# Performance work log

Hardware: AMD Instinct MI355X
Metric: run time of the kernel (lower is better)

Reference implementation:

```python
import jax, jax.numpy as jnp
import numpy as np

L, S, D = 2, 2048, 2048          # layers, seq_len, model dim
H, KVH, HD = 16, 4, 128          # heads, kv heads, head_dim (scale 128**0.5 is hardcoded in source)
F = 8192                         # ffn hidden
EPS = 1e-5
THETA = 500000.0                 # Llama-3 rope base


def setup_inputs() -> dict:
    key = jax.random.key(0)
    ks = jax.random.split(key, 9)
    sc = 0.02
    x = jax.random.normal(ks[0], (S, D), jnp.float32)
    inv_freq = 1.0 / (THETA ** (jnp.arange(0, HD, 2, dtype=jnp.float32) / HD))  # [HD/2]
    ang = jnp.arange(S, dtype=jnp.float32)[:, None] * inv_freq[None, :]         # [S, HD/2]
    w = lambda k, shape: jax.random.normal(k, shape, jnp.float32) * sc
    return {
        "token_embeddings_unnormal": x,
        "freqs_cos": jnp.cos(ang),
        "freqs_sin": jnp.sin(ang),
        "attn_norm_w": jnp.ones((L, D), jnp.float32),
        "wq": w(ks[1], (L, D, D)),
        "wk": w(ks[2], (L, KVH * HD, D)),
        "wv": w(ks[3], (L, KVH * HD, D)),
        "wo": w(ks[4], (L, D, D)),
        "ffn_norm_w": jnp.ones((L, D), jnp.float32),
        "w1": w(ks[5], (L, F, D)),
        "w2": w(ks[6], (L, D, F)),
        "w3": w(ks[7], (L, F, D)),
    }


def _rms_norm(x, w):
    # x * rsqrt(mean(x^2) + eps) * w  (matches source exactly)
    return x * jax.lax.rsqrt(jnp.mean(x * x, axis=-1, keepdims=True) + EPS) * w


def _rope(t, cos, sin):
    # t: [S, h, HD]; complex rotation of consecutive pairs by freqs_cis
    tp = t.reshape(t.shape[0], t.shape[1], HD // 2, 2)
    t0, t1 = tp[..., 0], tp[..., 1]
    c, s = cos[:, None, :], sin[:, None, :]
    return jnp.stack([t0 * c - t1 * s, t0 * s + t1 * c], axis=-1).reshape(t.shape)


def reference(token_embeddings_unnormal, freqs_cos, freqs_sin, attn_norm_w,
              wq, wk, wv, wo, ffn_norm_w, w1, w2, w3):
    x = token_embeddings_unnormal
    scale = 1.0 / np.sqrt(128.0)
    causal = jnp.tril(jnp.ones((S, S), bool))
    for l in range(L):
        h = _rms_norm(x, attn_norm_w[l])
        # batched per-head projections (source loops over heads; same math)
        q = jnp.einsum('sd,hed->she', h, wq[l].reshape(H, HD, D))
        k = jnp.einsum('sd,hed->she', h, wk[l].reshape(KVH, HD, D))
        v = jnp.einsum('sd,hed->she', h, wv[l].reshape(KVH, HD, D))
        q = _rope(q, freqs_cos, freqs_sin)
        k = _rope(k, freqs_cos, freqs_sin)
        # GQA: head `i` uses kv head i // 4
        k = jnp.repeat(k, H // KVH, axis=1)
        v = jnp.repeat(v, H // KVH, axis=1)
        scores = jnp.einsum('she,the->hst', q, k) * scale
        scores = jnp.where(causal[None], scores, -jnp.inf)
        probs = jax.nn.softmax(scores, axis=-1).astype(jnp.bfloat16).astype(jnp.float32)
        attn = jnp.einsum('hst,the->she', probs, v).reshape(S, H * HD)
        x = x + attn @ wo[l].T
        hf = _rms_norm(x, ffn_norm_w[l])
        x = x + (jax.nn.silu(hf @ w1[l].T) * (hf @ w3[l].T)) @ w2[l].T
    return x
```

## Files before the change

kernel.cpp:

```cpp
#include <hip/hip_runtime.h>

#define SLEN 2048
#define DM   2048
#define NH   16
#define NKVH 4
#define HD   128
#define KVD  512
#define FF   8192
#define NLAYER 2
#define EPSV 1e-5f

typedef unsigned short bhalf;
typedef __attribute__((__ext_vector_type__(8))) __bf16 bf16x8;
typedef __attribute__((__ext_vector_type__(4))) float f32x4;

__device__ __forceinline__ float b2f(bhalf u) {
  union { unsigned int i; float f; } v; v.i = ((unsigned int)u) << 16; return v.f;
}
__device__ __forceinline__ bhalf f2b(float f) {
  unsigned int x = __float_as_uint(f);
  return (bhalf)((x + 0x7fffu + ((x >> 16) & 1u)) >> 16);
}

typedef __attribute__((address_space(1))) const void gas_cvoid;
typedef __attribute__((address_space(3))) void las_void;
__device__ __forceinline__ void gload16(const void* g, void* l) {
  __builtin_amdgcn_global_load_lds((gas_cvoid*)g, (las_void*)l, 16, 0, 0);
}
__device__ __forceinline__ f32x4 mfma16(bf16x8 a, bf16x8 b, f32x4 c) {
  return __builtin_amdgcn_mfma_f32_16x16x32_bf16(a, b, c, 0, 0, 0);
}

__global__ __launch_bounds__(256)
void cvt_f32_bf16(const float* __restrict__ in, bhalf* __restrict__ out, size_t n) {
  size_t i = ((size_t)blockIdx.x * 256 + threadIdx.x) * 8;
  const size_t stride = (size_t)gridDim.x * 256 * 8;
  for (; i < n; i += stride) {
    float4 a = *(const float4*)(in + i);
    float4 b = *(const float4*)(in + i + 4);
    int4 o; bhalf* t = (bhalf*)&o;
    t[0]=f2b(a.x); t[1]=f2b(a.y); t[2]=f2b(a.z); t[3]=f2b(a.w);
    t[4]=f2b(b.x); t[5]=f2b(b.y); t[6]=f2b(b.z); t[7]=f2b(b.w);
    *(int4*)(out + i) = o;
  }
}

__global__ __launch_bounds__(256)
void rmsnorm_k(const float* __restrict__ x, const float* __restrict__ w,
               bhalf* __restrict__ out) {
  const int row = blockIdx.x;
  const int tid = threadIdx.x;
  const float4* xr = (const float4*)(x + (size_t)row * DM);
  float4 a = xr[tid*2], b = xr[tid*2 + 1];
  float ss = a.x*a.x + a.y*a.y + a.z*a.z + a.w*a.w
           + b.x*b.x + b.y*b.y + b.z*b.z + b.w*b.w;
  #pragma unroll
  for (int off = 32; off > 0; off >>= 1) ss += __shfl_down(ss, off);
  __shared__ float red[5];
  const int wv = tid >> 6, l = tid & 63;
  if (l == 0) red[wv] = ss;
  __syncthreads();
  if (tid == 0) red[4] = rsqrtf((red[0]+red[1]+red[2]+red[3]) * (1.0f/DM) + EPSV);
  __syncthreads();
  const float rs = red[4];
  const float* wp = w + tid*8;
  float vals[8] = {a.x,a.y,a.z,a.w,b.x,b.y,b.z,b.w};
  int4 o; bhalf* t = (bhalf*)&o;
  #pragma unroll
  for (int j = 0; j < 8; ++j) t[j] = f2b(vals[j] * rs * wp[j]);
  *(int4*)(out + (size_t)row*DM + tid*8) = o;
}

__global__ __launch_bounds__(256)
void rope_k(bhalf* __restrict__ t, const float* __restrict__ c,
            const float* __restrict__ s, int nheads) {
  const int idx = blockIdx.x * 256 + threadIdx.x;
  const int j  = idx & 63;
  const int hh = (idx >> 6) % nheads;
  const int sp = idx / (nheads * 64);
  const float cv = c[sp*64 + j], sv = s[sp*64 + j];
  unsigned int* p = (unsigned int*)(t + ((size_t)sp*nheads + hh)*HD + 2*j);
  const unsigned int pv = *p;
  const float t0 = b2f((bhalf)(pv & 0xffffu)), t1 = b2f((bhalf)(pv >> 16));
  const float o0 = t0*cv - t1*sv, o1 = t0*sv + t1*cv;
  *p = (unsigned int)f2b(o0) | ((unsigned int)f2b(o1) << 16);
}

template<int EPI>
__global__ __launch_bounds__(256, 2)
void gemm_bt(const bhalf* __restrict__ A, const bhalf* __restrict__ B,
             const int N, const int K,
             const bhalf* __restrict__ gate,
             float* __restrict__ outf, bhalf* __restrict__ outb) {
  __shared__ bhalf As[128*32];
  __shared__ bhalf Bs[128*32];
  const int tid = threadIdx.x;
  const int w = tid >> 6, l = tid & 63;
  const int l15 = l & 15, lg = l >> 4;
  const int ntn = N >> 7;
  const int nblocks = gridDim.x;
  const int qq = nblocks >> 3, rr = nblocks & 7;
  const int xcd = blockIdx.x & 7, loc = blockIdx.x >> 3;
  const int swz = (xcd < rr) ? (xcd*(qq+1) + loc) : (rr*(qq+1) + (xcd-rr)*qq + loc);
  const size_t m0 = (size_t)(swz / ntn) << 7;
  const size_t n0 = (size_t)(swz % ntn) << 7;
  f32x4 acc[4][4] = {};
  const int wr = w >> 1, wc = w & 1;
  const int stgrow = l >> 2;
  const int stgcol = (l & 3) << 3;
  const int nk = K >> 5;
  for (int kt = 0; kt < nk; ++kt) {
    const int k0 = kt << 5;
    #pragma unroll
    for (int it = 0; it < 2; ++it) {
      const int c = it*4 + w;
      const int row = c*16 + stgrow;
      gload16(&A[(m0 + row)*K + k0 + stgcol], &As[c*512]);
      gload16(&B[(n0 + row)*K + k0 + stgcol], &Bs[c*512]);
    }
    __syncthreads();
    bf16x8 af[4], bfr[4];
    #pragma unroll
    for (int m = 0; m < 4; ++m)
      af[m] = *(const bf16x8*)&As[(wr*64 + m*16 + l15)*32 + lg*8];
    #pragma unroll
    for (int n = 0; n < 4; ++n)
      bfr[n] = *(const bf16x8*)&Bs[(wc*64 + n*16 + l15)*32 + lg*8];
    #pragma unroll
    for (int m = 0; m < 4; ++m)
      #pragma unroll
      for (int n = 0; n < 4; ++n)
        acc[m][n] = mfma16(af[m], bfr[n], acc[m][n]);
    __syncthreads();
  }
  #pragma unroll
  for (int m = 0; m < 4; ++m) {
    const size_t row = m0 + wr*64 + m*16 + lg*4;
    #pragma unroll
    for (int n = 0; n < 4; ++n) {
      const size_t col = n0 + wc*64 + n*16 + l15;
      #pragma unroll
      for (int r2 = 0; r2 < 4; ++r2) {
        const size_t idx = (row + r2)*(size_t)N + col;
        const float v = acc[m][n][r2];
        if constexpr (EPI == 1) {
          outb[idx] = f2b(v);
        } else if constexpr (EPI == 2) {
          outf[idx] += v;
        } else {
          const float g = b2f(gate[idx]);
          const float si = g / (1.0f + __expf(-g));
          outb[idx] = f2b(si * v);
        }
      }
    }
  }
}

template<int EPI>
__global__ __launch_bounds__(512, 2)
void gemm256(const bhalf* __restrict__ A, const bhalf* __restrict__ B,
             const int N, const int lda, const int klen,
             const bhalf* __restrict__ gate, float* __restrict__ outf,
             bhalf* __restrict__ outb) {
  __shared__ __align__(16) bhalf As[3][256*32];
  __shared__ __align__(16) bhalf Bs[3][256*32];
  const int tid = threadIdx.x;
  const int w = tid >> 6, l = tid & 63;
  const int l15 = l & 15, lg = l >> 4;
  const int rdswz = (l15 >> 1) & 3;
  const int wr = w >> 2, wc = w & 3;
  const int ntn = N >> 8;
  const int nblocks = gridDim.x;
  const int qq = nblocks >> 3, rr = nblocks & 7;
  const int xcd = blockIdx.x & 7, loc = blockIdx.x >> 3;
  const int sb = (xcd < rr) ? (xcd*(qq+1) + loc) : (rr*(qq+1) + (xcd-rr)*qq + loc);
  const size_t m0 = (size_t)(sb / ntn) << 8;
  const size_t n0 = (size_t)(sb % ntn) << 8;
  const int k0 = blockIdx.y * klen;
  const int nk = klen >> 5;
  const int srow = l >> 2;
  const int scol = ((l & 3) ^ ((l >> 3) & 3)) << 3;
  const bhalf* Ag = A + m0 * (size_t)lda + k0;
  const bhalf* Bg = B + n0 * (size_t)lda + k0;

  auto stage = [&](int kt, int buf) {
    #pragma unroll
    for (int r = 0; r < 2; ++r) {
      const int chunk = r*8 + w;
      const size_t go = (size_t)(chunk*16 + srow)*lda + kt*32 + scol;
      gload16(Ag + go, &As[buf][chunk*512]);
      gload16(Bg + go, &Bs[buf][chunk*512]);
    }
  };

  f32x4 acc[8][4] = {};
  auto compute = [&](int cb) {
    const bhalf* Ab = As[cb];
    const bhalf* Bb = Bs[cb];
    const int co = (lg ^ rdswz) << 3;
    bf16x8 bfr[4], am[4];
    #pragma unroll
    for (int n = 0; n < 4; ++n)
      bfr[n] = *(const bf16x8*)&Bb[(wc*64 + n*16 + l15)*32 + co];
    #pragma unroll
    for (int m = 0; m < 4; ++m)
      am[m] = *(const bf16x8*)&Ab[(wr*128 + m*16 + l15)*32 + co];
    __builtin_amdgcn_s_setprio(1);
    #pragma unroll
    for (int m = 0; m < 4; ++m)
      #pragma unroll
      for (int n = 0; n < 4; ++n)
        acc[m][n] = mfma16(am[m], bfr[n], acc[m][n]);
    __builtin_amdgcn_s_setprio(0);
    #pragma unroll
    for (int m = 0; m < 4; ++m)
      am[m] = *(const bf16x8*)&Ab[(wr*128 + 64 + m*16 + l15)*32 + co];
    __builtin_amdgcn_s_setprio(1);
    #pragma unroll
    for (int m = 0; m < 4; ++m)
      #pragma unroll
      for (int n = 0; n < 4; ++n)
        acc[m + 4][n] = mfma16(am[m], bfr[n], acc[m + 4][n]);
    __builtin_amdgcn_s_setprio(0);
  };

  stage(0, 0);
  stage(1, 1);
  asm volatile("s_waitcnt vmcnt(4)" ::: "memory");
  __builtin_amdgcn_s_barrier();
  asm volatile("" ::: "memory");

  int cb = 0, pb = 2;
  for (int kt = 0; kt < nk - 2; ++kt) {
    stage(kt + 2, pb);
    compute(cb);
    asm volatile("s_waitcnt vmcnt(4)" ::: "memory");
    __builtin_amdgcn_s_barrier();
    asm volatile("" ::: "memory");
    cb = (cb + 1 == 3) ? 0 : cb + 1;
    pb = (pb + 1 == 3) ? 0 : pb + 1;
  }
  compute(cb);
  asm volatile("s_waitcnt vmcnt(0)" ::: "memory");
  __builtin_amdgcn_s_barrier();
  asm volatile("" ::: "memory");
  cb = (cb + 1 == 3) ? 0 : cb + 1;
  compute(cb);

  #pragma unroll
  for (int m = 0; m < 8; ++m) {
    const size_t row = m0 + wr*128 + m*16 + lg*4;
    #pragma unroll
    for (int n = 0; n < 4; ++n) {
      const size_t col = n0 + wc*64 + n*16 + l15;
      #pragma unroll
      for (int r2 = 0; r2 < 4; ++r2) {
        const size_t idx = (row + r2) * (size_t)N + col;
        const float v = acc[m][n][r2];
        if constexpr (EPI == 1) {
          outb[idx] = f2b(v);
        } else if constexpr (EPI == 2) {
          outf[idx] += v;
        } else if constexpr (EPI == 3) {
          const float g = b2f(gate[idx]);
          outb[idx] = f2b((g / (1.0f + __expf(-g))) * v);
        } else {
          atomicAdd(&outf[idx], v);
        }
      }
    }
  }
}

__global__ __launch_bounds__(256, 2)
void attn_k(const bhalf* __restrict__ qb, const bhalf* __restrict__ kb,
            const bhalf* __restrict__ vb, bhalf* __restrict__ ob) {
  __shared__ bhalf Ks[64][144];
  __shared__ bhalf Vt[128][80];
  __shared__ bhalf Ps[4][16][80];
  const int h  = blockIdx.x >> 5;
  const int qt = blockIdx.x & 31;
  const int kvh = h >> 2;
  const int tid = threadIdx.x;
  const int w = tid >> 6, l = tid & 63;
  const int l15 = l & 15, lg = l >> 4;
  const int q0 = qt << 6;

  bf16x8 qf[4];
  {
    const bhalf* qrow = qb + (size_t)(q0 + w*16 + l15)*DM + h*HD + lg*8;
    #pragma unroll
    for (int kc = 0; kc < 4; ++kc) qf[kc] = *(const bf16x8*)(qrow + kc*32);
  }
  float m_r[4] = {-3e38f,-3e38f,-3e38f,-3e38f};
  float l_r[4] = {0.f,0.f,0.f,0.f};
  f32x4 acc_o[8] = {};
  const float scale = 0.08838834764831845f;
  const int nt = qt + 1;
  for (int t = 0; t < nt; ++t) {
    const int k0 = t << 6;
    __syncthreads();
    #pragma unroll
    for (int it = 0; it < 4; ++it) {
      const int e = it*256 + tid;
      const int row = e >> 4;
      const int col = (e & 15) << 3;
      *(int4*)&Ks[row][col] =
          *(const int4*)(kb + (size_t)(k0 + row)*KVD + kvh*HD + col);
    }
    {
      const int d = tid & 127, g = tid >> 7;
      const bhalf* vp = vb + (size_t)(k0 + g*32)*KVD + kvh*HD + d;
      #pragma unroll
      for (int kk8 = 0; kk8 < 4; ++kk8) {
        int4 o; bhalf* tt = (bhalf*)&o;
        #pragma unroll
        for (int j2 = 0; j2 < 8; ++j2) tt[j2] = vp[(size_t)(kk8*8 + j2)*KVD];
        *(int4*)&Vt[d][g*32 + kk8*8] = o;
      }
    }
    __syncthreads();
    f32x4 sa[4] = {};
    #pragma unroll
    for (int kc = 0; kc < 4; ++kc)
      #pragma unroll
      for (int n = 0; n < 4; ++n) {
        bf16x8 kf = *(const bf16x8*)&Ks[n*16 + l15][kc*32 + lg*8];
        sa[n] = mfma16(qf[kc], kf, sa[n]);
      }
    const bool masked = (t == qt);
    #pragma unroll
    for (int r = 0; r < 4; ++r) {
      const int qg = q0 + w*16 + lg*4 + r;
      float sv[4];
      #pragma unroll
      for (int n = 0; n < 4; ++n) {
        float s = sa[n][r] * scale;
        if (masked && (k0 + n*16 + l15 > qg)) s = -3e38f;
        sv[n] = s;
      }
      float tm = fmaxf(fmaxf(sv[0], sv[1]), fmaxf(sv[2], sv[3]));
      tm = fmaxf(tm, __shfl_xor(tm, 1));
      tm = fmaxf(tm, __shfl_xor(tm, 2));
      tm = fmaxf(tm, __shfl_xor(tm, 4));
      tm = fmaxf(tm, __shfl_xor(tm, 8));
      const float mn = fmaxf(m_r[r], tm);
      const float alpha = __expf(m_r[r] - mn);
      float pv[4], psum = 0.f;
      #pragma unroll
      for (int n = 0; n < 4; ++n) { pv[n] = __expf(sv[n] - mn); psum += pv[n]; }
      psum += __shfl_xor(psum, 1);
      psum += __shfl_xor(psum, 2);
      psum += __shfl_xor(psum, 4);
      psum += __shfl_xor(psum, 8);
      l_r[r] = l_r[r]*alpha + psum;
      m_r[r] = mn;
      #pragma unroll
      for (int n2 = 0; n2 < 8; ++n2) acc_o[n2][r] *= alpha;
      #pragma unroll
      for (int n = 0; n < 4; ++n) Ps[w][lg*4 + r][n*16 + l15] = f2b(pv[n]);
    }
    #pragma unroll
    for (int kk = 0; kk < 2; ++kk) {
      bf16x8 pa = *(const bf16x8*)&Ps[w][l15][kk*32 + lg*8];
      #pragma unroll
      for (int n2 = 0; n2 < 8; ++n2) {
        bf16x8 vf = *(const bf16x8*)&Vt[n2*16 + l15][kk*32 + lg*8];
        acc_o[n2] = mfma16(pa, vf, acc_o[n2]);
      }
    }
  }
  #pragma unroll
  for (int r = 0; r < 4; ++r) {
    const float inv = 1.0f / l_r[r];
    bhalf* orow = ob + (size_t)(q0 + w*16 + lg*4 + r)*DM + h*HD;
    #pragma unroll
    for (int n2 = 0; n2 < 8; ++n2) orow[n2*16 + l15] = f2b(acc_o[n2][r] * inv);
  }
}

extern "C" void kernel_launch(void* const* d_in, const int* in_sizes, int n_in,
                              void* d_out, int out_size, void* d_ws, size_t ws_size,
                              hipStream_t stream) {
  (void)in_sizes; (void)n_in; (void)out_size; (void)ws_size;
  const float* x_in = (const float*)d_in[0];
  const float* fcos = (const float*)d_in[1];
  const float* fsin = (const float*)d_in[2];
  const float* anw  = (const float*)d_in[3];
  const float* wq   = (const float*)d_in[4];
  const float* wk   = (const float*)d_in[5];
  const float* wv   = (const float*)d_in[6];
  const float* wo   = (const float*)d_in[7];
  const float* fnw  = (const float*)d_in[8];
  const float* w1   = (const float*)d_in[9];
  const float* w2   = (const float*)d_in[10];
  const float* w3   = (const float*)d_in[11];
  float* x = (float*)d_out;

  char* p = (char*)d_ws;
  auto carve = [&](size_t elems) {
    bhalf* r = (bhalf*)p; p += ((elems*2 + 255) & ~(size_t)255); return r;
  };
  bhalf* wq_b = carve((size_t)NLAYER*DM*DM);
  bhalf* wk_b = carve((size_t)NLAYER*KVD*DM);
  bhalf* wv_b = carve((size_t)NLAYER*KVD*DM);
  bhalf* wo_b = carve((size_t)NLAYER*DM*DM);
  bhalf* w1_b = carve((size_t)NLAYER*FF*DM);
  bhalf* w2_b = carve((size_t)NLAYER*DM*FF);
  bhalf* w3_b = carve((size_t)NLAYER*FF*DM);
  bhalf* hn   = carve((size_t)SLEN*DM);
  bhalf* qb   = carve((size_t)SLEN*DM);
  bhalf* kb   = carve((size_t)SLEN*KVD);
  bhalf* vb   = carve((size_t)SLEN*KVD);
  bhalf* ab   = carve((size_t)SLEN*DM);
  bhalf* g1   = carve((size_t)SLEN*FF);

  hipMemcpyAsync(x, x_in, (size_t)SLEN*DM*sizeof(float),
                 hipMemcpyDeviceToDevice, stream);

  cvt_f32_bf16<<<2048,256,0,stream>>>(wq, wq_b, (size_t)NLAYER*DM*DM);
  cvt_f32_bf16<<<2048,256,0,stream>>>(wk, wk_b, (size_t)NLAYER*KVD*DM);
  cvt_f32_bf16<<<2048,256,0,stream>>>(wv, wv_b, (size_t)NLAYER*KVD*DM);
  cvt_f32_bf16<<<2048,256,0,stream>>>(wo, wo_b, (size_t)NLAYER*DM*DM);
  cvt_f32_bf16<<<2048,256,0,stream>>>(w1, w1_b, (size_t)NLAYER*FF*DM);
  cvt_f32_bf16<<<2048,256,0,stream>>>(w2, w2_b, (size_t)NLAYER*DM*FF);
  cvt_f32_bf16<<<2048,256,0,stream>>>(w3, w3_b, (size_t)NLAYER*FF*DM);

  for (int l = 0; l < NLAYER; ++l) {
    rmsnorm_k<<<SLEN,256,0,stream>>>(x, anw + l*DM, hn);
    gemm_bt<1><<<256,256,0,stream>>>(hn, wq_b + (size_t)l*DM*DM,  DM,  DM, nullptr, nullptr, qb);
    gemm_bt<1><<<64, 256,0,stream>>>(hn, wk_b + (size_t)l*KVD*DM, KVD, DM, nullptr, nullptr, kb);
    gemm_bt<1><<<64, 256,0,stream>>>(hn, wv_b + (size_t)l*KVD*DM, KVD, DM, nullptr, nullptr, vb);
    rope_k<<<SLEN*NH*64/256,  256,0,stream>>>(qb, fcos, fsin, NH);
    rope_k<<<SLEN*NKVH*64/256,256,0,stream>>>(kb, fcos, fsin, NKVH);
    attn_k<<<NH*(SLEN/64),256,0,stream>>>(qb, kb, vb, ab);
    gemm_bt<2><<<256,256,0,stream>>>(ab, wo_b + (size_t)l*DM*DM, DM, DM, nullptr, x, nullptr);
    rmsnorm_k<<<SLEN,256,0,stream>>>(x, fnw + l*DM, hn);
    gemm256<1><<<dim3((SLEN/256)*(FF/256),1),512,0,stream>>>(
        hn, w1_b + (size_t)l*FF*DM, FF, DM, DM, nullptr, nullptr, g1);
    gemm256<3><<<dim3((SLEN/256)*(FF/256),1),512,0,stream>>>(
        hn, w3_b + (size_t)l*FF*DM, FF, DM, DM, g1, nullptr, g1);
    gemm256<5><<<dim3((SLEN/256)*(DM/256),4),512,0,stream>>>(
        g1, w2_b + (size_t)l*DM*FF, DM, FF, FF/4, nullptr, x, nullptr);
  }
}
```

Measured before the change: 1.735 ms.

## Fuse Q/K/V projections into one GEMM and interleave staging in gemm256

Concatenates the Q, K and V weight matrices into a single 3072-wide bf16 buffer so one GEMM launch produces a packed QKV activation. Rope and attention are adjusted to read from this packed layout with row stride and offsets. Separately, the 256-tile GEMM now splits A and B tile loads and issues them between the two MFMA halves with extra barriers, aiming to spread memory issue across compute. The extra barriers add synchronisation cost, and the packed layout widens the strided V loads in attention.

```diff
diff --git a/kernel.cpp b/kernel.cpp
--- a/kernel.cpp
+++ b/kernel.cpp
@@ -9,6 +9,9 @@
 #define FF   8192
 #define NLAYER 2
 #define EPSV 1e-5f
+#define QKVW 3072
+#define KOFF 2048
+#define VOFF 2560
 
 typedef unsigned short bhalf;
 typedef __attribute__((__ext_vector_type__(8))) __bf16 bf16x8;
@@ -29,6 +32,11 @@
 }
 __device__ __forceinline__ f32x4 mfma16(bf16x8 a, bf16x8 b, f32x4 c) {
   return __builtin_amdgcn_mfma_f32_16x16x32_bf16(a, b, c, 0, 0, 0);
+}
+__device__ __forceinline__ void barrier_raw() {
+  asm volatile("" ::: "memory");
+  __builtin_amdgcn_s_barrier();
+  asm volatile("" ::: "memory");
 }
 
 __global__ __launch_bounds__(256)
@@ -73,13 +81,13 @@
 
 __global__ __launch_bounds__(256)
 void rope_k(bhalf* __restrict__ t, const float* __restrict__ c,
-            const float* __restrict__ s, int nheads) {
+            const float* __restrict__ s, int nheads, int rowstride, int off) {
   const int idx = blockIdx.x * 256 + threadIdx.x;
   const int j  = idx & 63;
   const int hh = (idx >> 6) % nheads;
   const int sp = idx / (nheads * 64);
   const float cv = c[sp*64 + j], sv = s[sp*64 + j];
-  unsigned int* p = (unsigned int*)(t + ((size_t)sp*nheads + hh)*HD + 2*j);
+  unsigned int* p = (unsigned int*)(t + (size_t)sp*rowstride + off + hh*HD + 2*j);
   const unsigned int pv = *p;
   const float t0 = b2f((bhalf)(pv & 0xffffu)), t1 = b2f((bhalf)(pv >> 16));
   const float o0 = t0*cv - t1*sv, o1 = t0*sv + t1*cv;
@@ -174,9 +182,9 @@
   const int nblocks = gridDim.x;
   const int qq = nblocks >> 3, rr = nblocks & 7;
   const int xcd = blockIdx.x & 7, loc = blockIdx.x >> 3;
-  const int sb = (xcd < rr) ? (xcd*(qq+1) + loc) : (rr*(qq+1) + (xcd-rr)*qq + loc);
-  const size_t m0 = (size_t)(sb / ntn) << 8;
-  const size_t n0 = (size_t)(sb % ntn) << 8;
+  const int sw = (xcd < rr) ? (xcd*(qq+1) + loc) : (rr*(qq+1) + (xcd-rr)*qq + loc);
+  const size_t m0 = (size_t)(sw / ntn) << 8;
+  const size_t n0 = (size_t)(sw % ntn) << 8;
   const int k0 = blockIdx.y * klen;
   const int nk = klen >> 5;
   const int srow = l >> 2;
@@ -184,21 +192,29 @@
   const bhalf* Ag = A + m0 * (size_t)lda + k0;
   const bhalf* Bg = B + n0 * (size_t)lda + k0;
 
-  auto stage = [&](int kt, int buf) {
+  auto stageA = [&](int kt, int bf) {
     #pragma unroll
     for (int r = 0; r < 2; ++r) {
       const int chunk = r*8 + w;
       const size_t go = (size_t)(chunk*16 + srow)*lda + kt*32 + scol;
-      gload16(Ag + go, &As[buf][chunk*512]);
-      gload16(Bg + go, &Bs[buf][chunk*512]);
+      gload16(Ag + go, &As[bf][chunk*512]);
     }
   };
+  auto stageB = [&](int kt, int bf) {
+    #pragma unroll
+    for (int r = 0; r < 2; ++r) {
+      const int chunk = r*8 + w;
+      const size_t go = (size_t)(chunk*16 + srow)*lda + kt*32 + scol;
+      gload16(Bg + go, &Bs[bf][chunk*512]);
+    }
+  };
 
   f32x4 acc[8][4] = {};
-  auto compute = [&](int cb) {
+  const int co = (lg ^ rdswz) << 3;
+
+  auto ktile = [&](int cb, int sbf, int kt2, bool stg) {
     const bhalf* Ab = As[cb];
     const bhalf* Bb = Bs[cb];
-    const int co = (lg ^ rdswz) << 3;
     bf16x8 bfr[4], am[4];
     #pragma unroll
     for (int n = 0; n < 4; ++n)
@@ -206,6 +222,8 @@
     #pragma unroll
     for (int m = 0; m < 4; ++m)
       am[m] = *(const bf16x8*)&Ab[(wr*128 + m*16 + l15)*32 + co];
+    if (stg) stageA(kt2, sbf);
+    barrier_raw();
     __builtin_amdgcn_s_setprio(1);
     #pragma unroll
     for (int m = 0; m < 4; ++m)
@@ -213,9 +231,12 @@
       for (int n = 0; n < 4; ++n)
         acc[m][n] = mfma16(am[m], bfr[n], acc[m][n]);
     __builtin_amdgcn_s_setprio(0);
+    barrier_raw();
     #pragma unroll
     for (int m = 0; m < 4; ++m)
       am[m] = *(const bf16x8*)&Ab[(wr*128 + 64 + m*16 + l15)*32 + co];
+    if (stg) stageB(kt2, sbf);
+    barrier_raw();
     __builtin_amdgcn_s_setprio(1);
     #pragma unroll
     for (int m = 0; m < 4; ++m)
@@ -225,28 +246,24 @@
     __builtin_amdgcn_s_setprio(0);
   };
 
-  stage(0, 0);
-  stage(1, 1);
+  stageA(0, 0); stageB(0, 0);
+  stageA(1, 1); stageB(1, 1);
   asm volatile("s_waitcnt vmcnt(4)" ::: "memory");
-  __builtin_amdgcn_s_barrier();
-  asm volatile("" ::: "memory");
-
-  int cb = 0, pb = 2;
+  barrier_raw();
+
+  int cb = 0;
   for (int kt = 0; kt < nk - 2; ++kt) {
-    stage(kt + 2, pb);
-    compute(cb);
+    const int sbf = (cb + 2 >= 3) ? cb - 1 : cb + 2;
+    ktile(cb, sbf, kt + 2, true);
     asm volatile("s_waitcnt vmcnt(4)" ::: "memory");
-    __builtin_amdgcn_s_barrier();
-    asm volatile("" ::: "memory");
+    barrier_raw();
     cb = (cb + 1 == 3) ? 0 : cb + 1;
-    pb = (pb + 1 == 3) ? 0 : pb + 1;
-  }
-  compute(cb);
+  }
+  ktile(cb, 0, 0, false);
   asm volatile("s_waitcnt vmcnt(0)" ::: "memory");
-  __builtin_amdgcn_s_barrier();
-  asm volatile("" ::: "memory");
+  barrier_raw();
   cb = (cb + 1 == 3) ? 0 : cb + 1;
-  compute(cb);
+  ktile(cb, 0, 0, false);
 
   #pragma unroll
   for (int m = 0; m < 8; ++m) {
@@ -274,8 +291,7 @@
 }
 
 __global__ __launch_bounds__(256, 2)
-void attn_k(const bhalf* __restrict__ qb, const bhalf* __restrict__ kb,
-            const bhalf* __restrict__ vb, bhalf* __restrict__ ob) {
+void attn_k(const bhalf* __restrict__ qkv, bhalf* __restrict__ ob) {
   __shared__ bhalf Ks[64][144];
   __shared__ bhalf Vt[128][80];
   __shared__ bhalf Ps[4][16][80];
@@ -289,7 +305,7 @@
 
   bf16x8 qf[4];
   {
-    const bhalf* qrow = qb + (size_t)(q0 + w*16 + l15)*DM + h*HD + lg*8;
+    const bhalf* qrow = qkv + (size_t)(q0 + w*16 + l15)*QKVW + h*HD + lg*8;
     #pragma unroll
     for (int kc = 0; kc < 4; ++kc) qf[kc] = *(const bf16x8*)(qrow + kc*32);
   }
@@ -307,16 +323,16 @@
       const int row = e >> 4;
       const int col = (e & 15) << 3;
       *(int4*)&Ks[row][col] =
-          *(const int4*)(kb + (size_t)(k0 + row)*KVD + kvh*HD + col);
+          *(const int4*)(qkv + (size_t)(k0 + row)*QKVW + KOFF + kvh*HD + col);
     }
     {
       const int d = tid & 127, g = tid >> 7;
-      const bhalf* vp = vb + (size_t)(k0 + g*32)*KVD + kvh*HD + d;
+      const bhalf* vp = qkv + (size_t)(k0 + g*32)*QKVW + VOFF + kvh*HD + d;
       #pragma unroll
       for (int kk8 = 0; kk8 < 4; ++kk8) {
         int4 o; bhalf* tt = (bhalf*)&o;
         #pragma unroll
-        for (int j2 = 0; j2 < 8; ++j2) tt[j2] = vp[(size_t)(kk8*8 + j2)*KVD];
+        for (int j2 = 0; j2 < 8; ++j2) tt[j2] = vp[(size_t)(kk8*8 + j2)*QKVW];
         *(int4*)&Vt[d][g*32 + kk8*8] = o;
       }
     }
@@ -402,26 +418,25 @@
   auto carve = [&](size_t elems) {
     bhalf* r = (bhalf*)p; p += ((elems*2 + 255) & ~(size_t)255); return r;
   };
-  bhalf* wq_b = carve((size_t)NLAYER*DM*DM);
-  bhalf* wk_b = carve((size_t)NLAYER*KVD*DM);
-  bhalf* wv_b = carve((size_t)NLAYER*KVD*DM);
+  bhalf* wqkv_b = carve((size_t)NLAYER*QKVW*DM);
   bhalf* wo_b = carve((size_t)NLAYER*DM*DM);
   bhalf* w1_b = carve((size_t)NLAYER*FF*DM);
   bhalf* w2_b = carve((size_t)NLAYER*DM*FF);
   bhalf* w3_b = carve((size_t)NLAYER*FF*DM);
   bhalf* hn   = carve((size_t)SLEN*DM);
-  bhalf* qb   = carve((size_t)SLEN*DM);
-  bhalf* kb   = carve((size_t)SLEN*KVD);
-  bhalf* vb   = carve((size_t)SLEN*KVD);
+  bhalf* qkv  = carve((size_t)SLEN*QKVW);
   bhalf* ab   = carve((size_t)SLEN*DM);
   bhalf* g1   = carve((size_t)SLEN*FF);
 
   hipMemcpyAsync(x, x_in, (size_t)SLEN*DM*sizeof(float),
                  hipMemcpyDeviceToDevice, stream);
 
-  cvt_f32_bf16<<<2048,256,0,stream>>>(wq, wq_b, (size_t)NLAYER*DM*DM);
-  cvt_f32_bf16<<<2048,256,0,stream>>>(wk, wk_b, (size_t)NLAYER*KVD*DM);
-  cvt_f32_bf16<<<2048,256,0,stream>>>(wv, wv_b, (size_t)NLAYER*KVD*DM);
+  for (int l = 0; l < NLAYER; ++l) {
+    bhalf* wb = wqkv_b + (size_t)l*QKVW*DM;
+    cvt_f32_bf16<<<1024,256,0,stream>>>(wq + (size_t)l*DM*DM,  wb,                    (size_t)DM*DM);
+    cvt_f32_bf16<<<512, 256,0,stream>>>(wk + (size_t)l*KVD*DM, wb + (size_t)KOFF*DM,  (size_t)KVD*DM);
+    cvt_f32_bf16<<<512, 256,0,stream>>>(wv + (size_t)l*KVD*DM, wb + (size_t)VOFF*DM,  (size_t)KVD*DM);
+  }
   cvt_f32_bf16<<<2048,256,0,stream>>>(wo, wo_b, (size_t)NLAYER*DM*DM);
   cvt_f32_bf16<<<2048,256,0,stream>>>(w1, w1_b, (size_t)NLAYER*FF*DM);
   cvt_f32_bf16<<<2048,256,0,stream>>>(w2, w2_b, (size_t)NLAYER*DM*FF);
@@ -429,12 +444,11 @@
 
   for (int l = 0; l < NLAYER; ++l) {
     rmsnorm_k<<<SLEN,256,0,stream>>>(x, anw + l*DM, hn);
-    gemm_bt<1><<<256,256,0,stream>>>(hn, wq_b + (size_t)l*DM*DM,  DM,  DM, nullptr, nullptr, qb);
-    gemm_bt<1><<<64, 256,0,stream>>>(hn, wk_b + (size_t)l*KVD*DM, KVD, DM, nullptr, nullptr, kb);
-    gemm_bt<1><<<64, 256,0,stream>>>(hn, wv_b + (size_t)l*KVD*DM, KVD, DM, nullptr, nullptr, vb);
-    rope_k<<<SLEN*NH*64/256,  256,0,stream>>>(qb, fcos, fsin, NH);
-    rope_k<<<SLEN*NKVH*64/256,256,0,stream>>>(kb, fcos, fsin, NKVH);
-    attn_k<<<NH*(SLEN/64),256,0,stream>>>(qb, kb, vb, ab);
+    gemm_bt<1><<<(SLEN/128)*(QKVW/128),256,0,stream>>>(
+        hn, wqkv_b + (size_t)l*QKVW*DM, QKVW, DM, nullptr, nullptr, qkv);
+    rope_k<<<SLEN*NH*64/256,  256,0,stream>>>(qkv, fcos, fsin, NH,   QKVW, 0);
+    rope_k<<<SLEN*NKVH*64/256,256,0,stream>>>(qkv, fcos, fsin, NKVH, QKVW, KOFF);
+    attn_k<<<NH*(SLEN/64),256,0,stream>>>(qkv, ab);
     gemm_bt<2><<<256,256,0,stream>>>(ab, wo_b + (size_t)l*DM*DM, DM, DM, nullptr, x, nullptr);
     rmsnorm_k<<<SLEN,256,0,stream>>>(x, fnw + l*DM, hn);
     gemm256<1><<<dim3((SLEN/256)*(FF/256),1),512,0,stream>>>(
```

Measured after the change: 1.550 ms. 10.6% less time.
